# Kernel optimization log

Measured on AMD Instinct MI355X. Metric: run time of the kernel, lower is better.

## Reference

```python
import jax, jax.numpy as jnp
import numpy as np

DIM = 1024
HEADS = 16
NEG = 1.0e10


def split_heads(v, heads):
    # Faithful to source: reshape puts heads LAST, then transpose -> [b, h, s, hd]
    b, s, d = v.shape
    hd = d // heads
    v = v.reshape(b, s, hd, heads)
    return jnp.transpose(v, (0, 3, 1, 2))


def merge_heads(v):
    b, h, s, hd = v.shape
    v = jnp.transpose(v, (0, 2, 3, 1))  # [b, s, hd, h]
    return v.reshape(b, s, h * hd)


def setup_inputs() -> dict:
    key = jax.random.key(0)
    kx, kq, kk, kv, ko = jax.random.split(key, 5)
    x = jax.random.normal(kx, (2, 2048, DIM), dtype=jnp.float32)
    # RandomNormal initializer default stddev 0.05
    qw = 0.05 * jax.random.normal(kq, (DIM, DIM), dtype=jnp.float32)
    kw = 0.05 * jax.random.normal(kk, (DIM, DIM), dtype=jnp.float32)
    vw = 0.05 * jax.random.normal(kv, (DIM, DIM), dtype=jnp.float32)
    ow = 0.05 * jax.random.normal(ko, (DIM, DIM), dtype=jnp.float32)
    return {"x": x, "qw": qw, "kw": kw, "vw": vw, "ow": ow}


def reference(x, qw, kw, vw, ow):
    b, s, d = x.shape
    Q = split_heads(x @ qw, HEADS)  # [b, h, s, hd]
    K = split_heads(x @ kw, HEADS)
    V = split_heads(x @ vw, HEADS)
    # NOTE: source scales by sqrt(dim), not sqrt(head_dim)
    score = jnp.einsum('bhqd,bhkd->bhqk', Q, K) / jnp.sqrt(jnp.float32(d))
    causal = jnp.tril(jnp.ones((1, 1, s, s), dtype=score.dtype))
    score = score - NEG * (1.0 - causal)
    weights = jax.nn.softmax(score, axis=-1)
    attn = jnp.einsum('bhqk,bhkd->bhqd', weights, V)
    return merge_heads(attn) @ ow
```

## Files before the change

kernel.cpp:

```cpp
#include <hip/hip_runtime.h>
#include <stdint.h>

typedef unsigned short ushort_t;
typedef __bf16 bf16x8 __attribute__((ext_vector_type(8)));
typedef float f32x4 __attribute__((ext_vector_type(4)));

#define DIM 1024
#define HEADS 16
#define HD 64
#define BATCH 2
#define SEQ 2048
#define MTOT (BATCH*SEQ)

#define C2F 0.045084220027780106f

__device__ __forceinline__ ushort_t f2bf(float f) {
    uint32_t u = __float_as_uint(f);
    uint32_t r = (u + 0x7FFFu + ((u >> 16) & 1u)) >> 16;
    return (ushort_t)r;
}

__device__ __forceinline__ uint32_t permpack(float lo, float hi) {
    return __builtin_amdgcn_perm(__float_as_uint(hi), __float_as_uint(lo), 0x07060302u);
}

__device__ __forceinline__ f32x4 mfma16(bf16x8 a, bf16x8 b, f32x4 c) {
    return __builtin_amdgcn_mfma_f32_16x16x32_bf16(a, b, c, 0, 0, 0);
}

__device__ __forceinline__ void glds16(const ushort_t* g, ushort_t* l) {
    __builtin_amdgcn_global_load_lds(
        (const __attribute__((address_space(1))) unsigned int*)g,
        (__attribute__((address_space(3))) unsigned int*)l, 16, 0, 0);
}

__global__ void k_prep(const float* __restrict__ x,
                       const float* __restrict__ w0, const float* __restrict__ w1,
                       const float* __restrict__ w2, const float* __restrict__ w3,
                       ushort_t* __restrict__ wt, ushort_t* __restrict__ xb) {
    const int z = blockIdx.z;
    int tx = threadIdx.x, ty = threadIdx.y;
    if (z == 4) {
        int bid = blockIdx.y * 32 + blockIdx.x;
        int t = ty * 32 + tx;
#pragma unroll
        for (int u = 0; u < 4; u++) {
            int i = bid * 1024 + u * 256 + t;
            const float4 v = ((const float4*)x)[i];
            ushort4 o;
            o.x = f2bf(v.x); o.y = f2bf(v.y); o.z = f2bf(v.z); o.w = f2bf(v.w);
            ((ushort4*)xb)[i] = o;
        }
        return;
    }
    __shared__ float t[32][33];
    const float* w = (z == 0) ? w0 : (z == 1) ? w1 : (z == 2) ? w2 : w3;
    ushort_t* o = wt + (size_t)z * DIM * DIM;
    int n0 = blockIdx.x * 32;
    int k0 = blockIdx.y * 32;
    if (z < 3) {
#pragma unroll
        for (int i = 0; i < 4; i++)
            t[ty + i * 8][tx] = w[(size_t)(k0 + ty + i * 8) * DIM + n0 + tx];
        __syncthreads();
#pragma unroll
        for (int i = 0; i < 4; i++) {
            int n = n0 + ty + i * 8;
            int np = (n & 15) * 64 + (n >> 4);
            o[(size_t)np * DIM + k0 + tx] = f2bf(t[tx][ty + i * 8]);
        }
    } else {
#pragma unroll
        for (int i = 0; i < 4; i++) {
            int kp = k0 + ty + i * 8;
            int k = (kp & 63) * 16 + (kp >> 6);
            t[ty + i * 8][tx] = w[(size_t)k * DIM + n0 + tx];
        }
        __syncthreads();
#pragma unroll
        for (int i = 0; i < 4; i++)
            o[(size_t)(n0 + ty + i * 8) * DIM + k0 + tx] = f2bf(t[tx][ty + i * 8]);
    }
}

__global__ __launch_bounds__(256) void k_qkv(const ushort_t* __restrict__ xb,
                                             const ushort_t* __restrict__ wt,
                                             ushort_t* __restrict__ qp,
                                             ushort_t* __restrict__ kp,
                                             ushort_t* __restrict__ vp) {
    __shared__ __align__(16) ushort_t lA[128 * 64];
    __shared__ __align__(16) ushort_t lB[128 * 64];
    const int z = blockIdx.z;
    const ushort_t* w = wt + (size_t)z * DIM * DIM;
    ushort_t* dst = (z == 0) ? qp : (z == 1) ? kp : vp;
    const float sc = (z == 0) ? C2F : 1.0f;
    const int tid = threadIdx.x;
    const int wave = tid >> 6;
    const int lane = tid & 63;
    const int l16 = lane & 15;
    const int quad = lane >> 4;
    const int m0 = blockIdx.x * 128;
    const int n0 = blockIdx.y * 128;
    const int mw = (wave & 1) * 64, nw = (wave >> 1) * 64;

    const f32x4 zero4 = {0.f, 0.f, 0.f, 0.f};
    f32x4 acc[4][4];
#pragma unroll
    for (int i = 0; i < 4; i++)
#pragma unroll
        for (int j = 0; j < 4; j++) acc[i][j] = zero4;

    const int swz = l16 & 7;
    for (int k0 = 0; k0 < DIM; k0 += 64) {
        __syncthreads();
#pragma unroll
        for (int j = 0; j < 4; j++) {
            int base = wave * 256 + j * 64;
            int L = base + lane;
            int row = L >> 3, cd = L & 7;
            int cs = cd ^ (row & 7);
            glds16(xb + (size_t)(m0 + row) * DIM + k0 + cs * 8, lA + base * 8);
            glds16(w + (size_t)(n0 + row) * DIM + k0 + cs * 8, lB + base * 8);
        }
        __syncthreads();
#pragma unroll
        for (int kk = 0; kk < 2; kk++) {
            bf16x8 a[4], b[4];
#pragma unroll
            for (int i = 0; i < 4; i++) {
                int rowa = mw + i * 16 + l16;
                int rowb = nw + i * 16 + l16;
                int ch = (kk * 4 + quad) ^ swz;
                a[i] = *(const bf16x8*)(lA + rowa * 64 + ch * 8);
                b[i] = *(const bf16x8*)(lB + rowb * 64 + ch * 8);
            }
#pragma unroll
            for (int ni = 0; ni < 4; ni++)
#pragma unroll
                for (int mi = 0; mi < 4; mi++)
                    acc[ni][mi] = mfma16(b[ni], a[mi], acc[ni][mi]);
        }
    }

#pragma unroll
    for (int ni = 0; ni < 4; ni++)
#pragma unroll
        for (int mi = 0; mi < 4; mi++) {
            int nbase = n0 + nw + ni * 16 + quad * 4;
            int m = m0 + mw + mi * 16 + l16;
            ushort4 o;
            o.x = f2bf(acc[ni][mi][0] * sc);
            o.y = f2bf(acc[ni][mi][1] * sc);
            o.z = f2bf(acc[ni][mi][2] * sc);
            o.w = f2bf(acc[ni][mi][3] * sc);
            *(ushort4*)(dst + (size_t)m * DIM + nbase) = o;
        }
}

__global__ void k_vt(const ushort_t* __restrict__ vp, ushort_t* __restrict__ vt) {
    __shared__ ushort_t t[32][34];
    const int bh = blockIdx.z, b = bh >> 4, h = bh & 15;
    const int s0 = blockIdx.x * 32;
    const int i0 = blockIdx.y * 32;
    int tx = threadIdx.x, ty = threadIdx.y;
#pragma unroll
    for (int j = 0; j < 4; j++)
        t[ty + j * 8][tx] = vp[(size_t)(b * SEQ + s0 + ty + j * 8) * DIM + h * HD + i0 + tx];
    __syncthreads();
#pragma unroll
    for (int j = 0; j < 4; j++)
        vt[((size_t)bh * HD + i0 + ty + j * 8) * SEQ + s0 + tx] = t[tx][ty + j * 8];
}

__global__ __launch_bounds__(256) void k_attn(const ushort_t* __restrict__ qp,
                                              const ushort_t* __restrict__ kp,
                                              const ushort_t* __restrict__ vt,
                                              ushort_t* __restrict__ mg) {
    __shared__ __align__(16) ushort_t lK[2][64 * 64];
    __shared__ __align__(16) ushort_t lV[2][64 * 64];
    __shared__ __align__(16) ushort_t lP[4][16 * 72];
    const int tid = threadIdx.x;
    const int w = tid >> 6;
    const int lane = tid & 63;
    const int l16 = lane & 15;
    const int quad = lane >> 4;
    const int bh = blockIdx.y, b = bh >> 4, h = bh & 15;

    const ushort_t* Q = qp + (size_t)b * SEQ * DIM + h * HD;
    const ushort_t* K = kp + (size_t)b * SEQ * DIM + h * HD;
    const ushort_t* V = vt + (size_t)bh * HD * SEQ;

    const int swz = l16 & 7;
    ushort_t* pw = lP[w] + l16 * 72;

    union { ushort_t u[8]; bf16x8 v; } one8;
#pragma unroll
    for (int j = 0; j < 8; j++) one8.u[j] = 0x3F80;

#pragma unroll 1
    for (int phase = 0; phase < 2; phase++) {
        const int qi = phase ? (31 - (int)blockIdx.x) : (int)blockIdx.x;
        const int qb = qi * 64;
        const int mb = qb + w * 16;
        const int nt = qi + 1;

        bf16x8 qf[2];
#pragma unroll
        for (int hf = 0; hf < 2; hf++)
            qf[hf] = *(const bf16x8*)(Q + (size_t)(mb + l16) * DIM + hf * 32 + quad * 8);

        const f32x4 zero4 = {0.f, 0.f, 0.f, 0.f};
        f32x4 oT[4];
#pragma unroll
        for (int nb = 0; nb < 4; nb++) oT[nb] = zero4;
        f32x4 ls = zero4;

        __syncthreads();
#pragma unroll
        for (int j = 0; j < 2; j++) {
            int base = w * 128 + j * 64;
            int L = base + lane;
            int row = L >> 3, cd = L & 7;
            int cs = cd ^ (row & 7);
            glds16(K + (size_t)row * DIM + cs * 8, lK[0] + base * 8);
            glds16(V + (size_t)row * SEQ + cs * 8, lV[0] + base * 8);
        }

        int cur = 0;
        for (int kt = 0; kt < nt; kt++) {
            const int kb = kt * 64;
            __syncthreads();
            if (kt + 1 < nt) {
                const int kb2 = kb + 64;
#pragma unroll
                for (int j = 0; j < 2; j++) {
                    int base = w * 128 + j * 64;
                    int L = base + lane;
                    int row = L >> 3, cd = L & 7;
                    int cs = cd ^ (row & 7);
                    glds16(K + (size_t)(kb2 + row) * DIM + cs * 8, lK[cur ^ 1] + base * 8);
                    glds16(V + (size_t)row * SEQ + kb2 + cs * 8, lV[cur ^ 1] + base * 8);
                }
            }

            bf16x8 kf[4][2], vf[4][2];
#pragma unroll
            for (int c = 0; c < 4; c++)
#pragma unroll
                for (int hf = 0; hf < 2; hf++) {
                    int row = c * 16 + l16;
                    int ch = (hf * 4 + quad) ^ swz;
                    kf[c][hf] = *(const bf16x8*)(lK[cur] + row * 64 + ch * 8);
                }
#pragma unroll
            for (int nb = 0; nb < 4; nb++)
#pragma unroll
                for (int pr = 0; pr < 2; pr++) {
                    int row = nb * 16 + l16;
                    int ch = (pr * 4 + quad) ^ swz;
                    vf[nb][pr] = *(const bf16x8*)(lV[cur] + row * 64 + ch * 8);
                }

            f32x4 s4[4];
#pragma unroll
            for (int c = 0; c < 4; c++) {
                f32x4 t = zero4;
                t = mfma16(kf[c][0], qf[0], t);
                t = mfma16(kf[c][1], qf[1], t);
                s4[c] = t;
            }

            const bool needmask = (kt == nt - 1);
            const int qrow = mb + l16;
#pragma unroll
            for (int c = 0; c < 4; c++) {
                float e0 = exp2f(s4[c][0]);
                float e1 = exp2f(s4[c][1]);
                float e2 = exp2f(s4[c][2]);
                float e3 = exp2f(s4[c][3]);
                if (needmask) {
                    int k = kb + c * 16 + quad * 4;
                    if (k + 0 > qrow) e0 = 0.f;
                    if (k + 1 > qrow) e1 = 0.f;
                    if (k + 2 > qrow) e2 = 0.f;
                    if (k + 3 > qrow) e3 = 0.f;
                }
                *(uint32_t*)(pw + c * 16 + quad * 4) = permpack(e0, e1);
                *(uint32_t*)(pw + c * 16 + quad * 4 + 2) = permpack(e2, e3);
            }
            bf16x8 pa[2];
#pragma unroll
            for (int pr = 0; pr < 2; pr++)
                pa[pr] = *(const bf16x8*)(pw + pr * 32 + quad * 8);

#pragma unroll
            for (int nb = 0; nb < 4; nb++) {
                oT[nb] = mfma16(vf[nb][0], pa[0], oT[nb]);
                oT[nb] = mfma16(vf[nb][1], pa[1], oT[nb]);
            }
            ls = mfma16(one8.v, pa[0], ls);
            ls = mfma16(one8.v, pa[1], ls);
            cur ^= 1;
        }

        float inv = 1.0f / ls[0];
        int srow = mb + l16;
#pragma unroll
        for (int nb = 0; nb < 4; nb++) {
            ushort4 o;
            o.x = f2bf(oT[nb][0] * inv);
            o.y = f2bf(oT[nb][1] * inv);
            o.z = f2bf(oT[nb][2] * inv);
            o.w = f2bf(oT[nb][3] * inv);
            *(ushort4*)(mg + ((size_t)b * SEQ + srow) * DIM + h * HD + nb * 16 + quad * 4) = o;
        }
    }
}

__global__ __launch_bounds__(256) void k_out(const ushort_t* __restrict__ a_in,
                                             const ushort_t* __restrict__ wt,
                                             float* __restrict__ out) {
    __shared__ __align__(16) ushort_t lA[128 * 64];
    __shared__ __align__(16) ushort_t lB[128 * 64];
    const int tid = threadIdx.x;
    const int wave = tid >> 6;
    const int lane = tid & 63;
    const int l16 = lane & 15;
    const int quad = lane >> 4;
    const int m0 = blockIdx.x * 128;
    const int n0 = blockIdx.y * 128;
    const int mw = (wave & 1) * 64, nw = (wave >> 1) * 64;

    const f32x4 zero4 = {0.f, 0.f, 0.f, 0.f};
    f32x4 acc[4][4];
#pragma unroll
    for (int i = 0; i < 4; i++)
#pragma unroll
        for (int j = 0; j < 4; j++) acc[i][j] = zero4;

    const int swz = l16 & 7;
    for (int k0 = 0; k0 < DIM; k0 += 64) {
        __syncthreads();
#pragma unroll
        for (int j = 0; j < 4; j++) {
            int base = wave * 256 + j * 64;
            int L = base + lane;
            int row = L >> 3, cd = L & 7;
            int cs = cd ^ (row & 7);
            glds16(a_in + (size_t)(m0 + row) * DIM + k0 + cs * 8, lA + base * 8);
            glds16(wt + (size_t)(n0 + row) * DIM + k0 + cs * 8, lB + base * 8);
        }
        __syncthreads();
#pragma unroll
        for (int kk = 0; kk < 2; kk++) {
            bf16x8 a[4], b[4];
#pragma unroll
            for (int i = 0; i < 4; i++) {
                int rowa = mw + i * 16 + l16;
                int rowb = nw + i * 16 + l16;
                int ch = (kk * 4 + quad) ^ swz;
                a[i] = *(const bf16x8*)(lA + rowa * 64 + ch * 8);
                b[i] = *(const bf16x8*)(lB + rowb * 64 + ch * 8);
            }
#pragma unroll
            for (int ni = 0; ni < 4; ni++)
#pragma unroll
                for (int mi = 0; mi < 4; mi++)
                    acc[ni][mi] = mfma16(b[ni], a[mi], acc[ni][mi]);
        }
    }

#pragma unroll
    for (int ni = 0; ni < 4; ni++)
#pragma unroll
        for (int mi = 0; mi < 4; mi++) {
            int nbase = n0 + nw + ni * 16 + quad * 4;
            int m = m0 + mw + mi * 16 + l16;
            *(float4*)(out + (size_t)m * DIM + nbase) = *(float4*)&acc[ni][mi];
        }
}

extern "C" void kernel_launch(void* const* d_in, const int* in_sizes, int n_in,
                              void* d_out, int out_size, void* d_ws, size_t ws_size,
                              hipStream_t stream) {
    const float* x  = (const float*)d_in[0];
    const float* qw = (const float*)d_in[1];
    const float* kw = (const float*)d_in[2];
    const float* vw = (const float*)d_in[3];
    const float* ow = (const float*)d_in[4];
    float* out = (float*)d_out;

    ushort_t* xb = (ushort_t*)d_ws;
    ushort_t* wt = xb + (size_t)MTOT * DIM;
    ushort_t* qp = wt + (size_t)4 * DIM * DIM;
    ushort_t* kp = qp + (size_t)MTOT * DIM;
    ushort_t* vp = kp + (size_t)MTOT * DIM;
    ushort_t* vt = vp + (size_t)MTOT * DIM;
    ushort_t* mg = xb;

    k_prep<<<dim3(32, 32, 5), dim3(32, 8), 0, stream>>>(x, qw, kw, vw, ow, wt, xb);
    k_qkv<<<dim3(MTOT / 128, DIM / 128, 3), dim3(256), 0, stream>>>(xb, wt, qp, kp, vp);
    k_vt<<<dim3(SEQ / 32, HD / 32, BATCH * HEADS), dim3(32, 8), 0, stream>>>(vp, vt);
    k_attn<<<dim3(SEQ / 128, BATCH * HEADS), dim3(256), 0, stream>>>(qp, kp, vt, mg);
    k_out<<<dim3(MTOT / 128, DIM / 128), dim3(256), 0, stream>>>(mg, wt + (size_t)3 * DIM * DIM, out);
}
```

Baseline: 188.2 us.

## Double attention KV tile to 128 rows and halve out-projection M tile

The attention kernel now stages 128 keys and values per iteration instead of 64. Each tile is processed as two 64-key halves, and halves lying wholly beyond the wave's causal limit are skipped. This halves the number of barriers and prefetch rounds per query block, at the cost of doubling LDS use, which may lower occupancy. The V tile uses a 16-way XOR swizzle to match its wider rows. Separately, the output projection GEMM switches to 64x128 tiles, doubling its grid to improve CU fill, at the cost of less reuse of the weight tile.

```diff
diff --git a/kernel.cpp b/kernel.cpp
--- a/kernel.cpp
+++ b/kernel.cpp
@@ -176,8 +176,8 @@
                                               const ushort_t* __restrict__ kp,
                                               const ushort_t* __restrict__ vt,
                                               ushort_t* __restrict__ mg) {
-    __shared__ __align__(16) ushort_t lK[2][64 * 64];
-    __shared__ __align__(16) ushort_t lV[2][64 * 64];
+    __shared__ __align__(16) ushort_t lK[2][128 * 64];
+    __shared__ __align__(16) ushort_t lV[2][64 * 128];
     __shared__ __align__(16) ushort_t lP[4][16 * 72];
     const int tid = threadIdx.x;
     const int w = tid >> 6;
@@ -191,6 +191,7 @@
     const ushort_t* V = vt + (size_t)bh * HD * SEQ;
 
     const int swz = l16 & 7;
+    const int swzv = l16;
     ushort_t* pw = lP[w] + l16 * 72;
 
     union { ushort_t u[8]; bf16x8 v; } one8;
@@ -202,7 +203,7 @@
         const int qi = phase ? (31 - (int)blockIdx.x) : (int)blockIdx.x;
         const int qb = qi * 64;
         const int mb = qb + w * 16;
-        const int nt = qi + 1;
+        const int nt = (qb >> 7) + 1;
 
         bf16x8 qf[2];
 #pragma unroll
@@ -217,89 +218,97 @@
 
         __syncthreads();
 #pragma unroll
-        for (int j = 0; j < 2; j++) {
-            int base = w * 128 + j * 64;
+        for (int j = 0; j < 4; j++) {
+            int base = w * 256 + j * 64;
             int L = base + lane;
-            int row = L >> 3, cd = L & 7;
-            int cs = cd ^ (row & 7);
-            glds16(K + (size_t)row * DIM + cs * 8, lK[0] + base * 8);
-            glds16(V + (size_t)row * SEQ + cs * 8, lV[0] + base * 8);
+            int rk = L >> 3, ck = L & 7;
+            glds16(K + (size_t)rk * DIM + (ck ^ (rk & 7)) * 8, lK[0] + base * 8);
+            int rv = L >> 4, cv = L & 15;
+            glds16(V + (size_t)rv * SEQ + (cv ^ (rv & 15)) * 8, lV[0] + base * 8);
         }
 
         int cur = 0;
         for (int kt = 0; kt < nt; kt++) {
-            const int kb = kt * 64;
+            const int kb = kt * 128;
             __syncthreads();
             if (kt + 1 < nt) {
-                const int kb2 = kb + 64;
-#pragma unroll
-                for (int j = 0; j < 2; j++) {
-                    int base = w * 128 + j * 64;
+                const int kb2 = kb + 128;
+#pragma unroll
+                for (int j = 0; j < 4; j++) {
+                    int base = w * 256 + j * 64;
                     int L = base + lane;
-                    int row = L >> 3, cd = L & 7;
-                    int cs = cd ^ (row & 7);
-                    glds16(K + (size_t)(kb2 + row) * DIM + cs * 8, lK[cur ^ 1] + base * 8);
-                    glds16(V + (size_t)row * SEQ + kb2 + cs * 8, lV[cur ^ 1] + base * 8);
+                    int rk = L >> 3, ck = L & 7;
+                    glds16(K + (size_t)(kb2 + rk) * DIM + (ck ^ (rk & 7)) * 8,
+                           lK[cur ^ 1] + base * 8);
+                    int rv = L >> 4, cv = L & 15;
+                    glds16(V + (size_t)rv * SEQ + kb2 + (cv ^ (rv & 15)) * 8,
+                           lV[cur ^ 1] + base * 8);
                 }
             }
 
-            bf16x8 kf[4][2], vf[4][2];
-#pragma unroll
-            for (int c = 0; c < 4; c++)
-#pragma unroll
-                for (int hf = 0; hf < 2; hf++) {
-                    int row = c * 16 + l16;
-                    int ch = (hf * 4 + quad) ^ swz;
-                    kf[c][hf] = *(const bf16x8*)(lK[cur] + row * 64 + ch * 8);
+#pragma unroll
+            for (int half = 0; half < 2; half++) {
+                const int kh = kb + half * 64;
+                if (kh > mb + 15) continue;
+
+                bf16x8 kf[4][2], vf[4][2];
+#pragma unroll
+                for (int c = 0; c < 4; c++)
+#pragma unroll
+                    for (int hf = 0; hf < 2; hf++) {
+                        int row = half * 64 + c * 16 + l16;
+                        int ch = (hf * 4 + quad) ^ swz;
+                        kf[c][hf] = *(const bf16x8*)(lK[cur] + row * 64 + ch * 8);
+                    }
+#pragma unroll
+                for (int nb = 0; nb < 4; nb++)
+#pragma unroll
+                    for (int pr = 0; pr < 2; pr++) {
+                        int row = nb * 16 + l16;
+                        int ch = (half * 8 + pr * 4 + quad) ^ swzv;
+                        vf[nb][pr] = *(const bf16x8*)(lV[cur] + row * 128 + ch * 8);
+                    }
+
+                f32x4 s4[4];
+#pragma unroll
+                for (int c = 0; c < 4; c++) {
+                    f32x4 t = zero4;
+                    t = mfma16(kf[c][0], qf[0], t);
+                    t = mfma16(kf[c][1], qf[1], t);
+                    s4[c] = t;
                 }
-#pragma unroll
-            for (int nb = 0; nb < 4; nb++)
-#pragma unroll
-                for (int pr = 0; pr < 2; pr++) {
-                    int row = nb * 16 + l16;
-                    int ch = (pr * 4 + quad) ^ swz;
-                    vf[nb][pr] = *(const bf16x8*)(lV[cur] + row * 64 + ch * 8);
+
+                const bool needmask = (kh + 63 > mb);
+                const int qrow = mb + l16;
+#pragma unroll
+                for (int c = 0; c < 4; c++) {
+                    float e0 = exp2f(s4[c][0]);
+                    float e1 = exp2f(s4[c][1]);
+                    float e2 = exp2f(s4[c][2]);
+                    float e3 = exp2f(s4[c][3]);
+                    if (needmask) {
+                        int k = kh + c * 16 + quad * 4;
+                        if (k + 0 > qrow) e0 = 0.f;
+                        if (k + 1 > qrow) e1 = 0.f;
+                        if (k + 2 > qrow) e2 = 0.f;
+                        if (k + 3 > qrow) e3 = 0.f;
+                    }
+                    *(uint32_t*)(pw + c * 16 + quad * 4) = permpack(e0, e1);
+                    *(uint32_t*)(pw + c * 16 + quad * 4 + 2) = permpack(e2, e3);
                 }
-
-            f32x4 s4[4];
-#pragma unroll
-            for (int c = 0; c < 4; c++) {
-                f32x4 t = zero4;
-                t = mfma16(kf[c][0], qf[0], t);
-                t = mfma16(kf[c][1], qf[1], t);
-                s4[c] = t;
+                bf16x8 pa[2];
+#pragma unroll
+                for (int pr = 0; pr < 2; pr++)
+                    pa[pr] = *(const bf16x8*)(pw + pr * 32 + quad * 8);
+
+#pragma unroll
+                for (int nb = 0; nb < 4; nb++) {
+                    oT[nb] = mfma16(vf[nb][0], pa[0], oT[nb]);
+                    oT[nb] = mfma16(vf[nb][1], pa[1], oT[nb]);
+                }
+                ls = mfma16(one8.v, pa[0], ls);
+                ls = mfma16(one8.v, pa[1], ls);
             }
-
-            const bool needmask = (kt == nt - 1);
-            const int qrow = mb + l16;
-#pragma unroll
-            for (int c = 0; c < 4; c++) {
-                float e0 = exp2f(s4[c][0]);
-                float e1 = exp2f(s4[c][1]);
-                float e2 = exp2f(s4[c][2]);
-                float e3 = exp2f(s4[c][3]);
-                if (needmask) {
-                    int k = kb + c * 16 + quad * 4;
-                    if (k + 0 > qrow) e0 = 0.f;
-                    if (k + 1 > qrow) e1 = 0.f;
-                    if (k + 2 > qrow) e2 = 0.f;
-                    if (k + 3 > qrow) e3 = 0.f;
-                }
-                *(uint32_t*)(pw + c * 16 + quad * 4) = permpack(e0, e1);
-                *(uint32_t*)(pw + c * 16 + quad * 4 + 2) = permpack(e2, e3);
-            }
-            bf16x8 pa[2];
-#pragma unroll
-            for (int pr = 0; pr < 2; pr++)
-                pa[pr] = *(const bf16x8*)(pw + pr * 32 + quad * 8);
-
-#pragma unroll
-            for (int nb = 0; nb < 4; nb++) {
-                oT[nb] = mfma16(vf[nb][0], pa[0], oT[nb]);
-                oT[nb] = mfma16(vf[nb][1], pa[1], oT[nb]);
-            }
-            ls = mfma16(one8.v, pa[0], ls);
-            ls = mfma16(one8.v, pa[1], ls);
             cur ^= 1;
         }
 
@@ -320,52 +329,63 @@
 __global__ __launch_bounds__(256) void k_out(const ushort_t* __restrict__ a_in,
                                              const ushort_t* __restrict__ wt,
                                              float* __restrict__ out) {
-    __shared__ __align__(16) ushort_t lA[128 * 64];
+    __shared__ __align__(16) ushort_t lA[64 * 64];
     __shared__ __align__(16) ushort_t lB[128 * 64];
     const int tid = threadIdx.x;
     const int wave = tid >> 6;
     const int lane = tid & 63;
     const int l16 = lane & 15;
     const int quad = lane >> 4;
-    const int m0 = blockIdx.x * 128;
+    const int m0 = blockIdx.x * 64;
     const int n0 = blockIdx.y * 128;
-    const int mw = (wave & 1) * 64, nw = (wave >> 1) * 64;
+    const int mw = (wave & 1) * 32, nw = (wave >> 1) * 64;
 
     const f32x4 zero4 = {0.f, 0.f, 0.f, 0.f};
-    f32x4 acc[4][4];
+    f32x4 acc[4][2];
 #pragma unroll
     for (int i = 0; i < 4; i++)
 #pragma unroll
-        for (int j = 0; j < 4; j++) acc[i][j] = zero4;
+        for (int j = 0; j < 2; j++) acc[i][j] = zero4;
 
     const int swz = l16 & 7;
     for (int k0 = 0; k0 < DIM; k0 += 64) {
         __syncthreads();
+#pragma unroll
+        for (int j = 0; j < 2; j++) {
+            int base = wave * 128 + j * 64;
+            int L = base + lane;
+            int row = L >> 3, cd = L & 7;
+            int cs = cd ^ (row & 7);
+            glds16(a_in + (size_t)(m0 + row) * DIM + k0 + cs * 8, lA + base * 8);
+        }
 #pragma unroll
         for (int j = 0; j < 4; j++) {
             int base = wave * 256 + j * 64;
             int L = base + lane;
             int row = L >> 3, cd = L & 7;
             int cs = cd ^ (row & 7);
-            glds16(a_in + (size_t)(m0 + row) * DIM + k0 + cs * 8, lA + base * 8);
             glds16(wt + (size_t)(n0 + row) * DIM + k0 + cs * 8, lB + base * 8);
         }
         __syncthreads();
 #pragma unroll
         for (int kk = 0; kk < 2; kk++) {
-            bf16x8 a[4], b[4];
+            bf16x8 a[2], b[4];
+#pragma unroll
+            for (int i = 0; i < 2; i++) {
+                int rowa = mw + i * 16 + l16;
+                int ch = (kk * 4 + quad) ^ swz;
+                a[i] = *(const bf16x8*)(lA + rowa * 64 + ch * 8);
+            }
 #pragma unroll
             for (int i = 0; i < 4; i++) {
-                int rowa = mw + i * 16 + l16;
                 int rowb = nw + i * 16 + l16;
                 int ch = (kk * 4 + quad) ^ swz;
-                a[i] = *(const bf16x8*)(lA + rowa * 64 + ch * 8);
                 b[i] = *(const bf16x8*)(lB + rowb * 64 + ch * 8);
             }
 #pragma unroll
             for (int ni = 0; ni < 4; ni++)
 #pragma unroll
-                for (int mi = 0; mi < 4; mi++)
+                for (int mi = 0; mi < 2; mi++)
                     acc[ni][mi] = mfma16(b[ni], a[mi], acc[ni][mi]);
         }
     }
@@ -373,7 +393,7 @@
 #pragma unroll
     for (int ni = 0; ni < 4; ni++)
 #pragma unroll
-        for (int mi = 0; mi < 4; mi++) {
+        for (int mi = 0; mi < 2; mi++) {
             int nbase = n0 + nw + ni * 16 + quad * 4;
             int m = m0 + mw + mi * 16 + l16;
             *(float4*)(out + (size_t)m * DIM + nbase) = *(float4*)&acc[ni][mi];
@@ -402,5 +422,5 @@
     k_qkv<<<dim3(MTOT / 128, DIM / 128, 3), dim3(256), 0, stream>>>(xb, wt, qp, kp, vp);
     k_vt<<<dim3(SEQ / 32, HD / 32, BATCH * HEADS), dim3(32, 8), 0, stream>>>(vp, vt);
     k_attn<<<dim3(SEQ / 128, BATCH * HEADS), dim3(256), 0, stream>>>(qp, kp, vt, mg);
-    k_out<<<dim3(MTOT / 128, DIM / 128), dim3(256), 0, stream>>>(mg, wt + (size_t)3 * DIM * DIM, out);
-}
+    k_out<<<dim3(MTOT / 64, DIM / 128), dim3(256), 0, stream>>>(mg, wt + (size_t)3 * DIM * DIM, out);
+}
```

Measured after the change: 191.1 us. About the same (+1.5%).
